# Optimization experiments

Hardware: AMD Instinct MI355X
Metric: run time of the kernel (lower is better)

## Reference

```python
import jax, jax.numpy as jnp
import numpy as np

BS = 4  # gating blocksize


def setup_inputs() -> dict:
    key = jax.random.key(0)
    k1, k2, k3 = jax.random.split(key, 3)
    batch, rows, width, cols = 8, 2048, 4096, 4096
    X = jax.random.normal(k1, (batch, rows, width), dtype=jnp.float32)
    W = jax.random.normal(k2, (width, cols), dtype=jnp.float32)
    G = jax.random.normal(k3, (batch, width // BS, cols // BS), dtype=jnp.float32)
    return {"X": X, "W": W, "G": G}


def _gmm(X, W, G):
    # Y[b,r,c] = sum_k X[b,r,k] * W[k,c] * G[b, k//BS, c//BS]
    b = X.shape[0]
    # expand block gates to elementwise resolution
    Gf = jnp.repeat(jnp.repeat(G, BS, axis=1), BS, axis=2)  # (b, width, cols)
    # per-batch gated weight, then batched GEMM
    return jnp.einsum('brk,kc,bkc->brc', X, W, Gf)


def reference(X, W, G):
    Y = _gmm(X, W, G)
    s = Y.sum()
    return s * s
```

## Files before the change

### kernel.cpp

```cpp
#include <hip/hip_runtime.h>

#define BATCH 8
#define ROWS  2048
#define WIDTH 4096
#define COLS  4096
#define KB    1024
#define CB    1024
#define RCH   64

__global__ __launch_bounds__(256) void colsum_kernel(const float4* __restrict__ X,
                                                     float* __restrict__ xs) {
    const int k4 = blockIdx.x * blockDim.x + threadIdx.x;
    const int b  = blockIdx.y;
    const int r0 = blockIdx.z * RCH;

    const float4* p = X + (size_t)(b * ROWS + r0) * (WIDTH / 4) + k4;
    float ax = 0.f, ay = 0.f, az = 0.f, aw = 0.f;
#pragma unroll 8
    for (int r = 0; r < RCH; ++r) {
        float4 v = p[(size_t)r * (WIDTH / 4)];
        ax += v.x; ay += v.y; az += v.z; aw += v.w;
    }
    float* dst = xs + (size_t)b * WIDTH + 4 * k4;
    atomicAdd(dst + 0, ax);
    atomicAdd(dst + 1, ay);
    atomicAdd(dst + 2, az);
    atomicAdd(dst + 3, aw);
}

__global__ __launch_bounds__(256) void gated_reduce_kernel(const float* __restrict__ W,
                                                           const float* __restrict__ G,
                                                           const float* __restrict__ xs,
                                                           float* __restrict__ blocksum) {
    const int cb = blockIdx.x * blockDim.x + threadIdx.x;
    const int kb = blockIdx.y;

    const float4* Wv = (const float4*)W;
    float w4[4];
#pragma unroll
    for (int j = 0; j < 4; ++j) {
        float4 w = Wv[(size_t)(4 * kb + j) * CB + cb];
        w4[j] = (w.x + w.y) + (w.z + w.w);
    }

    float acc = 0.f;
#pragma unroll
    for (int b = 0; b < BATCH; ++b) {
        float inner = 0.f;
#pragma unroll
        for (int j = 0; j < 4; ++j)
            inner += xs[b * WIDTH + 4 * kb + j] * w4[j];
        acc += G[((size_t)b * KB + kb) * CB + cb] * inner;
    }

    __shared__ float red[256];
    red[threadIdx.x] = acc;
    __syncthreads();
    for (int off = 128; off > 0; off >>= 1) {
        if (threadIdx.x < off) red[threadIdx.x] += red[threadIdx.x + off];
        __syncthreads();
    }
    if (threadIdx.x == 0)
        blocksum[blockIdx.y * gridDim.x + blockIdx.x] = red[0];
}

__global__ __launch_bounds__(256) void finalize_kernel(const float* __restrict__ blocksum,
                                                       int n, float* __restrict__ out) {
    float acc = 0.f;
    for (int i = threadIdx.x; i < n; i += 256) acc += blocksum[i];
    __shared__ float red[256];
    red[threadIdx.x] = acc;
    __syncthreads();
    for (int off = 128; off > 0; off >>= 1) {
        if (threadIdx.x < off) red[threadIdx.x] += red[threadIdx.x + off];
        __syncthreads();
    }
    if (threadIdx.x == 0) {
        float s = red[0];
        out[0] = s * s;
    }
}

extern "C" void kernel_launch(void* const* d_in, const int* in_sizes, int n_in,
                              void* d_out, int out_size, void* d_ws, size_t ws_size,
                              hipStream_t stream) {
    const float* X = (const float*)d_in[0];
    const float* W = (const float*)d_in[1];
    const float* G = (const float*)d_in[2];
    float* out = (float*)d_out;

    float* xs       = (float*)d_ws;
    float* blocksum = xs + BATCH * WIDTH;
    const int nblocksum = (CB / 256) * KB;

    hipMemsetAsync(d_ws, 0, (size_t)BATCH * WIDTH * sizeof(float), stream);

    dim3 g1(WIDTH / 4 / 256, BATCH, ROWS / RCH);
    colsum_kernel<<<g1, 256, 0, stream>>>((const float4*)X, xs);

    dim3 g2(CB / 256, KB);
    gated_reduce_kernel<<<g2, 256, 0, stream>>>(W, G, xs, blocksum);

    finalize_kernel<<<1, 256, 0, stream>>>(blocksum, nblocksum, out);
}
```

Baseline: 89.08 us.

## Decouple W·G reduction from X column sums and run both in one kernel

The sum is rewritten as sum_b,k xs[b,k]*wg[b,k], where wg is the gated W row-sum reduced over columns. Its computation no longer depends on xs, so it runs concurrently with the X column-sum in a single launch, with odd and even blocks taking the two roles. A small final kernel forms the dot product. This removes the serial dependency between the two memory-bound passes and one kernel launch. The cost is a heavier wg block, with 32 accumulators per thread and wave-shuffle reductions.

```diff
diff --git a/kernel.cpp b/kernel.cpp
--- a/kernel.cpp
+++ b/kernel.cpp
@@ -8,71 +8,86 @@
 #define CB    1024
 #define RCH   64
 
-__global__ __launch_bounds__(256) void colsum_kernel(const float4* __restrict__ X,
-                                                     float* __restrict__ xs) {
-    const int k4 = blockIdx.x * blockDim.x + threadIdx.x;
-    const int b  = blockIdx.y;
-    const int r0 = blockIdx.z * RCH;
+__global__ __launch_bounds__(256) void fused_kernel(const float4* __restrict__ Xv,
+                                                    const float4* __restrict__ Wv,
+                                                    const float* __restrict__ G,
+                                                    float* __restrict__ xs,
+                                                    float* __restrict__ wg) {
+    const int tid = threadIdx.x;
+    if (blockIdx.x & 1) {
+        const int kb = blockIdx.x >> 1;
+        float acc[8][4];
+#pragma unroll
+        for (int b = 0; b < 8; ++b)
+#pragma unroll
+            for (int j = 0; j < 4; ++j) acc[b][j] = 0.f;
 
-    const float4* p = X + (size_t)(b * ROWS + r0) * (WIDTH / 4) + k4;
-    float ax = 0.f, ay = 0.f, az = 0.f, aw = 0.f;
+#pragma unroll
+        for (int chunk = 0; chunk < CB / 256; ++chunk) {
+            const int cb = chunk * 256 + tid;
+            float w4[4];
+#pragma unroll
+            for (int j = 0; j < 4; ++j) {
+                float4 w = Wv[(size_t)(4 * kb + j) * CB + cb];
+                w4[j] = (w.x + w.y) + (w.z + w.w);
+            }
+#pragma unroll
+            for (int b = 0; b < 8; ++b) {
+                float g = G[((size_t)b * KB + kb) * CB + cb];
+#pragma unroll
+                for (int j = 0; j < 4; ++j) acc[b][j] += g * w4[j];
+            }
+        }
+
+        __shared__ float lds[4][32];
+        const int lane = tid & 63, wid = tid >> 6;
+#pragma unroll
+        for (int v = 0; v < 32; ++v) {
+            float x = acc[v >> 2][v & 3];
+#pragma unroll
+            for (int o = 1; o < 64; o <<= 1) x += __shfl_xor(x, o, 64);
+            if (lane == 0) lds[wid][v] = x;
+        }
+        __syncthreads();
+        if (tid < 32) {
+            float r = lds[0][tid] + lds[1][tid] + lds[2][tid] + lds[3][tid];
+            const int b = tid >> 2, j = tid & 3;
+            wg[(size_t)b * WIDTH + 4 * kb + j] = r;
+        }
+    } else {
+        const int c  = blockIdx.x >> 1;
+        const int k4 = (c & 3) * 256 + tid;
+        const int b  = (c >> 2) & 7;
+        const int r0 = (c >> 5) * RCH;
+
+        const float4* p = Xv + (size_t)(b * ROWS + r0) * (WIDTH / 4) + k4;
+        float ax = 0.f, ay = 0.f, az = 0.f, aw = 0.f;
 #pragma unroll 8
-    for (int r = 0; r < RCH; ++r) {
-        float4 v = p[(size_t)r * (WIDTH / 4)];
-        ax += v.x; ay += v.y; az += v.z; aw += v.w;
+        for (int r = 0; r < RCH; ++r) {
+            float4 v = p[(size_t)r * (WIDTH / 4)];
+            ax += v.x; ay += v.y; az += v.z; aw += v.w;
+        }
+        float* dst = xs + (size_t)b * WIDTH + 4 * k4;
+        atomicAdd(dst + 0, ax);
+        atomicAdd(dst + 1, ay);
+        atomicAdd(dst + 2, az);
+        atomicAdd(dst + 3, aw);
     }
-    float* dst = xs + (size_t)b * WIDTH + 4 * k4;
-    atomicAdd(dst + 0, ax);
-    atomicAdd(dst + 1, ay);
-    atomicAdd(dst + 2, az);
-    atomicAdd(dst + 3, aw);
 }
 
-__global__ __launch_bounds__(256) void gated_reduce_kernel(const float* __restrict__ W,
-                                                           const float* __restrict__ G,
-                                                           const float* __restrict__ xs,
-                                                           float* __restrict__ blocksum) {
-    const int cb = blockIdx.x * blockDim.x + threadIdx.x;
-    const int kb = blockIdx.y;
-
-    const float4* Wv = (const float4*)W;
-    float w4[4];
-#pragma unroll
-    for (int j = 0; j < 4; ++j) {
-        float4 w = Wv[(size_t)(4 * kb + j) * CB + cb];
-        w4[j] = (w.x + w.y) + (w.z + w.w);
+__global__ __launch_bounds__(256) void final_kernel(const float4* __restrict__ xs4,
+                                                    const float4* __restrict__ wg4,
+                                                    float* __restrict__ out) {
+    float acc = 0.f;
+    for (int i = threadIdx.x; i < BATCH * WIDTH / 4; i += 256) {
+        float4 a = xs4[i], b = wg4[i];
+        acc += a.x * b.x + a.y * b.y + a.z * b.z + a.w * b.w;
     }
-
-    float acc = 0.f;
-#pragma unroll
-    for (int b = 0; b < BATCH; ++b) {
-        float inner = 0.f;
-#pragma unroll
-        for (int j = 0; j < 4; ++j)
-            inner += xs[b * WIDTH + 4 * kb + j] * w4[j];
-        acc += G[((size_t)b * KB + kb) * CB + cb] * inner;
-    }
-
     __shared__ float red[256];
     red[threadIdx.x] = acc;
     __syncthreads();
-    for (int off = 128; off > 0; off >>= 1) {
-        if (threadIdx.x < off) red[threadIdx.x] += red[threadIdx.x + off];
-        __syncthreads();
-    }
-    if (threadIdx.x == 0)
-        blocksum[blockIdx.y * gridDim.x + blockIdx.x] = red[0];
-}
-
-__global__ __launch_bounds__(256) void finalize_kernel(const float* __restrict__ blocksum,
-                                                       int n, float* __restrict__ out) {
-    float acc = 0.f;
-    for (int i = threadIdx.x; i < n; i += 256) acc += blocksum[i];
-    __shared__ float red[256];
-    red[threadIdx.x] = acc;
-    __syncthreads();
-    for (int off = 128; off > 0; off >>= 1) {
-        if (threadIdx.x < off) red[threadIdx.x] += red[threadIdx.x + off];
+    for (int o = 128; o > 0; o >>= 1) {
+        if (threadIdx.x < o) red[threadIdx.x] += red[threadIdx.x + o];
         __syncthreads();
     }
     if (threadIdx.x == 0) {
@@ -89,17 +104,12 @@
     const float* G = (const float*)d_in[2];
     float* out = (float*)d_out;
 
-    float* xs       = (float*)d_ws;
-    float* blocksum = xs + BATCH * WIDTH;
-    const int nblocksum = (CB / 256) * KB;
+    float* xs = (float*)d_ws;
+    float* wg = xs + BATCH * WIDTH;
 
-    hipMemsetAsync(d_ws, 0, (size_t)BATCH * WIDTH * sizeof(float), stream);
+    hipMemsetAsync(xs, 0, (size_t)BATCH * WIDTH * sizeof(float), stream);
 
-    dim3 g1(WIDTH / 4 / 256, BATCH, ROWS / RCH);
-    colsum_kernel<<<g1, 256, 0, stream>>>((const float4*)X, xs);
+    fused_kernel<<<2048, 256, 0, stream>>>((const float4*)X, (const float4*)W, G, xs, wg);
 
-    dim3 g2(CB / 256, KB);
-    gated_reduce_kernel<<<g2, 256, 0, stream>>>(W, G, xs, blocksum);
-
-    finalize_kernel<<<1, 256, 0, stream>>>(blocksum, nblocksum, out);
+    final_kernel<<<1, 256, 0, stream>>>((const float4*)xs, (const float4*)wg, out);
 }
```

After: 90.79 us. About the same (+1.9%).
